# Performance work log

Hardware: AMD Instinct MI355X
Metric: run time of the kernel (lower is better)

Reference implementation:

```python
import jax, jax.numpy as jnp
import numpy as np

D_MODEL = 2048
D_STATE = 128
D_CONV = 4
NHEADS = 64
NGROUPS = 1
HEAD_DIM = 64
CHUNK = 128
EPS = 1e-5
D_INNER = NHEADS * HEAD_DIM                       # 4096
CONV_DIM = D_INNER + 2 * NGROUPS * D_STATE        # 4352
D_IN_PROJ = 2 * D_INNER + 2 * NGROUPS * D_STATE + NHEADS  # 8512


def setup_inputs() -> dict:
    key = jax.random.key(0)
    ks = jax.random.split(key, 9)
    B, S = 2, 4096
    return dict(
        hidden_states=jax.random.normal(ks[0], (B, S, D_MODEL), jnp.float32),
        W_in=jax.random.normal(ks[1], (D_MODEL, D_IN_PROJ), jnp.float32) * 0.02,
        conv_w=jax.random.normal(ks[2], (CONV_DIM, D_CONV), jnp.float32) * 0.2,
        conv_b=jax.random.normal(ks[3], (CONV_DIM,), jnp.float32) * 0.1,
        # A must be negative (stable SSM): A = -exp(u), u ~ U[0,2)
        A=-jnp.exp(jax.random.uniform(ks[4], (NHEADS,), jnp.float32, 0.0, 2.0)),
        D=jax.random.normal(ks[5], (NHEADS,), jnp.float32),
        dt_bias=jax.random.normal(ks[6], (NHEADS,), jnp.float32),
        norm_w=jnp.ones((D_INNER,), jnp.float32),
        W_out=jax.random.normal(ks[7], (D_INNER, D_MODEL), jnp.float32) * 0.02,
    )


def _silu(x):
    return x * jax.nn.sigmoid(x)


def _causal_conv1d(x, w, b):
    # depthwise causal conv with silu; x [B,S,C], w [C,K], b [C]
    K = w.shape[1]
    S = x.shape[1]
    xp = jnp.pad(x, ((0, 0), (K - 1, 0), (0, 0)))
    y = sum(xp[:, k:k + S, :] * w[None, None, :, k].swapaxes(-1, -1) for k in range(0))
    y = jnp.zeros_like(x)
    for k in range(K):
        y = y + xp[:, k:k + S, :] * w[:, k][None, None, :]
    return _silu(y + b)


def _ssd(x, dt, A, Bm, Cm, chunk):
    # Mamba2 chunked SSD scan.
    # x [b,s,h,p]; dt [b,s,h] (>0); A [h]; Bm,Cm [b,s,g,n]
    b, s, h, p = x.shape
    g, n = Bm.shape[2], Bm.shape[3]
    hh = h // g
    c = s // chunk
    x = x.reshape(b, c, chunk, g, hh, p)
    dt = dt.reshape(b, c, chunk, g, hh)
    Bm = Bm.reshape(b, c, chunk, g, n)
    Cm = Cm.reshape(b, c, chunk, g, n)
    dA = dt * A.reshape(g, hh)                 # [b,c,l,g,hh]
    dA_cs = jnp.cumsum(dA, axis=2)             # [b,c,l,g,hh]
    dtx = dt[..., None] * x                    # [b,c,l,g,hh,p]
    # intra-chunk (diagonal blocks): L[i,j] = exp(sum_{j<k<=i} dA)
    diff = dA_cs[:, :, :, None] - dA_cs[:, :, None, :]   # [b,c,i,j,g,hh]
    mask = jnp.tril(jnp.ones((chunk, chunk), bool))
    L = jnp.exp(jnp.where(mask[None, None, :, :, None, None], diff, -jnp.inf))
    Y = jnp.einsum('bcign,bcjgn,bcijgh,bcjghp->bcighp', Cm, Bm, L, dtx)
    # chunk-final states
    decay = jnp.exp(dA_cs[:, :, -1:] - dA_cs)            # [b,c,l,g,hh]
    states = jnp.einsum('bcjgn,bcjgh,bcjghp->bcghpn', Bm, decay, dtx)
    chunk_decay = jnp.exp(dA_cs[:, :, -1])               # [b,c,g,hh]
    def step(prev, inp):
        cd, st = inp
        return cd[..., None, None] * prev + st, prev
    init = jnp.zeros_like(states[:, 0])
    _, prevs = jax.lax.scan(step, init,
                            (jnp.moveaxis(chunk_decay, 1, 0), jnp.moveaxis(states, 1, 0)))
    prevs = jnp.moveaxis(prevs, 0, 1)                    # [b,c,g,hh,p,n] state entering each chunk
    Y = Y + jnp.einsum('bcign,bcghpn,bcigh->bcighp', Cm, prevs, jnp.exp(dA_cs))
    return Y.reshape(b, s, h, p)


def reference(hidden_states, W_in, conv_w, conv_b, A, D, dt_bias, norm_w, W_out):
    Bsz, S, _ = hidden_states.shape
    zxbcdt = hidden_states @ W_in                        # [B,S,d_in_proj]
    z = zxbcdt[..., :D_INNER]
    xbc = zxbcdt[..., D_INNER:D_INNER + CONV_DIM]
    dt = zxbcdt[..., D_INNER + CONV_DIM:]                # [B,S,nheads]
    xbc = _causal_conv1d(xbc, conv_w, conv_b)            # silu-activated causal conv
    x = xbc[..., :D_INNER].reshape(Bsz, S, NHEADS, HEAD_DIM)
    Bm = xbc[..., D_INNER:D_INNER + NGROUPS * D_STATE].reshape(Bsz, S, NGROUPS, D_STATE)
    Cm = xbc[..., D_INNER + NGROUPS * D_STATE:].reshape(Bsz, S, NGROUPS, D_STATE)
    dt = jax.nn.softplus(dt + dt_bias)                   # delta_softplus, dt_limit=(0,inf)
    y = _ssd(x, dt, A, Bm, Cm, CHUNK)
    y = y + D[None, None, :, None] * x                   # skip (D) term
    y = y.reshape(Bsz, S, D_INNER)
    # gated RMSNorm (norm_before_gate=False): normalize(y * silu(z)), grouped
    yg = y * _silu(z)
    gsz = D_INNER // NGROUPS
    ygr = yg.reshape(Bsz, S, NGROUPS, gsz)
    rms = jax.lax.rsqrt(jnp.mean(ygr * ygr, axis=-1, keepdims=True) + EPS)
    yn = (ygr * rms).reshape(Bsz, S, D_INNER) * norm_w
    return yn @ W_out
```

## Files before the change

### kernel.cpp

```cpp
#include <hip/hip_runtime.h>
#include <hip/hip_bf16.h>

typedef __bf16 bf16_t;
typedef bf16_t bf16x8 __attribute__((ext_vector_type(8)));
typedef float f32x4 __attribute__((ext_vector_type(4)));

#define TOK 8192
#define DMODEL 2048
#define DINNER 4096
#define XBCN 4352
#define DSTATE 128
#define NH 64
#define HD 64
#define NBC 64
#define WINT_ROWS 8448

__device__ __forceinline__ void gld16(const bf16_t* g, bf16_t* l) {
  __builtin_amdgcn_global_load_lds((const __attribute__((address_space(1))) void*)g,
                                   (__attribute__((address_space(3))) void*)l, 16, 0, 0);
}

__device__ __forceinline__ f32x4 mfma16(bf16x8 a, bf16x8 b, f32x4 c) {
  return __builtin_amdgcn_mfma_f32_16x16x32_bf16(a, b, c, 0, 0, 0);
}

__device__ __forceinline__ bf16x8 ldsr(unsigned addr) {
  f32x4 r;
  asm volatile("ds_read_b128 %0, %1" : "=v"(r) : "v"(addr));
  return __builtin_bit_cast(bf16x8, r);
}


__global__ __launch_bounds__(256)
void cast_split_kernel(const float* __restrict__ in, bf16_t* __restrict__ hi,
                       bf16_t* __restrict__ lo, size_t n) {
  size_t i = ((size_t)blockIdx.x * 256 + threadIdx.x) * 8;
  if (i + 8 > n) return;
  float4 a = *(const float4*)(in + i);
  float4 b = *(const float4*)(in + i + 4);
  float v[8] = {a.x,a.y,a.z,a.w,b.x,b.y,b.z,b.w};
  bf16x8 h, l;
#pragma unroll
  for (int j = 0; j < 8; ++j) {
    h[j] = (bf16_t)v[j];
    l[j] = (bf16_t)(v[j] - (float)h[j]);
  }
  *(bf16x8*)(hi + i) = h;
  *(bf16x8*)(lo + i) = l;
}

__global__ __launch_bounds__(256)
void transpose_cast_kernel(const float* __restrict__ in, bf16_t* __restrict__ out,
                           int R, int C, int outRows) {
  __shared__ float tile[32][33];
  const int c0 = blockIdx.x * 32;
  const int r0 = blockIdx.y * 32;
  const int tx = threadIdx.x & 31;
  const int ty = threadIdx.x >> 5;
#pragma unroll
  for (int k = 0; k < 4; ++k) {
    int r = r0 + ty + k*8;
    int c = c0 + tx;
    tile[ty + k*8][tx] = (c < C) ? in[(size_t)r * C + c] : 0.f;
  }
  __syncthreads();
#pragma unroll
  for (int k = 0; k < 4; ++k) {
    int oc = c0 + ty + k*8;
    int orr = r0 + tx;
    out[(size_t)oc * R + orr] = (bf16_t)tile[tx][ty + k*8];
  }
}

__global__ __launch_bounds__(256)
void wdt_split_kernel(const float* __restrict__ Win, bf16_t* __restrict__ Whi,
                      bf16_t* __restrict__ Wlo) {
  const int h = threadIdx.x & 63;
  const int k0 = blockIdx.x * 256 + (threadIdx.x >> 6) * 64;
#pragma unroll 4
  for (int i = 0; i < 64; ++i) {
    int k = k0 + i;
    float v = Win[(size_t)k * 8512 + 8448 + h];
    bf16_t hv = (bf16_t)v;
    Whi[(size_t)h * DMODEL + k] = hv;
    Wlo[(size_t)h * DMODEL + k] = (bf16_t)(v - (float)hv);
  }
}

template <typename OutT>
__global__ __launch_bounds__(512, 2)
void gemm256(const bf16_t* __restrict__ A, const bf16_t* __restrict__ B,
             OutT* __restrict__ C0, OutT* __restrict__ C1,
             long M, long N, long K, long splitN, int gridX) {
  __shared__ bf16_t sA[2][2][8192];
  __shared__ bf16_t sB[2][2][8192];
  const int tid = threadIdx.x;
  const int lane = tid & 63;
  const int wid = tid >> 6;
  const int wr = wid >> 2;
  const int wc = wid & 3;

  const int x = blockIdx.x & 7;
  const int q = blockIdx.x >> 3;
  const long bm = (long)(x * 4 + (q & 3)) * 256;
  const long bn = (long)(q >> 2) * 256;

  const int srow = (wid >> 1) * 16 + (lane & 15);
  const int skof = (wid & 1) * 32 + (lane >> 4) * 8;
  const bf16_t* Abase = A + (bm + srow) * K + skof;
  const bf16_t* Bbase = B + (bn + srow) * K + skof;

  auto stageA = [&](int buf, int h, long kt) {
    const bf16_t* s = Abase + (long)h * 128 * K + kt;
    gld16(s,          &sA[buf][h][wid * 512]);
    gld16(s + 64 * K, &sA[buf][h][4096 + wid * 512]);
  };
  auto stageB = [&](int buf, int h, long kt) {
    const bf16_t* s = Bbase + (long)h * 128 * K + kt;
    gld16(s,          &sB[buf][h][wid * 512]);
    gld16(s + 64 * K, &sB[buf][h][4096 + wid * 512]);
  };

  const unsigned sAb = (unsigned)(uintptr_t)(__attribute__((address_space(3))) void*)&sA[0][0][0]
                       + (unsigned)lane * 16 + (unsigned)wr * 8192;
  const unsigned sBb = (unsigned)(uintptr_t)(__attribute__((address_space(3))) void*)&sB[0][0][0]
                       + (unsigned)lane * 16 + (unsigned)wc * 4096;

  stageA(0, 0, 0); stageB(0, 0, 0); stageB(0, 1, 0); stageA(0, 1, 0);

  f32x4 acc[8][4] = {};
  bf16x8 a0[4][2], a1[4][2], b0[2][2], b1[2][2];
  int cur = 0;
  const int NT = (int)(K >> 6);

  for (int t = 0; t < NT; ++t) {
    const bool fin = (t == NT - 1);
    const long ktn = (long)(t + 1) * 64;
    const unsigned ab = sAb + (unsigned)cur * 32768;
    const unsigned bb = sBb + (unsigned)cur * 32768;

    asm volatile("s_waitcnt vmcnt(0)\n\ts_barrier" ::: "memory");

    if (!fin) {
      stageA(cur ^ 1, 0, ktn);
      stageB(cur ^ 1, 0, ktn);
      stageB(cur ^ 1, 1, ktn);
      stageA(cur ^ 1, 1, ktn);
    }
    __builtin_amdgcn_sched_barrier(0);

#pragma unroll
    for (int mi = 0; mi < 4; ++mi) {
      a0[mi][0] = ldsr(ab + (mi*2+0)*1024);
      a0[mi][1] = ldsr(ab + (mi*2+1)*1024);
    }
#pragma unroll
    for (int ni = 0; ni < 2; ++ni) {
      b0[ni][0] = ldsr(bb + (ni*2+0)*1024);
      b0[ni][1] = ldsr(bb + (ni*2+1)*1024);
    }
#pragma unroll
    for (int ni = 0; ni < 2; ++ni) {
      b1[ni][0] = ldsr(bb + 16384 + (ni*2+0)*1024);
      b1[ni][1] = ldsr(bb + 16384 + (ni*2+1)*1024);
    }
#pragma unroll
    for (int mi = 0; mi < 4; ++mi) {
      a1[mi][0] = ldsr(ab + 16384 + (mi*2+0)*1024);
      a1[mi][1] = ldsr(ab + 16384 + (mi*2+1)*1024);
    }
    __builtin_amdgcn_sched_barrier(0);

    asm volatile("s_waitcnt lgkmcnt(12)" ::: "memory");
    __builtin_amdgcn_sched_barrier(0);
    __builtin_amdgcn_s_setprio(1);
#pragma unroll
    for (int mi = 0; mi < 4; ++mi)
#pragma unroll
      for (int ni = 0; ni < 2; ++ni) {
        acc[mi][ni] = mfma16(a0[mi][0], b0[ni][0], acc[mi][ni]);
        acc[mi][ni] = mfma16(a0[mi][1], b0[ni][1], acc[mi][ni]);
      }
    __builtin_amdgcn_s_setprio(0);
    __builtin_amdgcn_sched_barrier(0);

    asm volatile("s_waitcnt lgkmcnt(8)" ::: "memory");
    __builtin_amdgcn_sched_barrier(0);
    __builtin_amdgcn_s_setprio(1);
#pragma unroll
    for (int mi = 0; mi < 4; ++mi)
#pragma unroll
      for (int ni = 0; ni < 2; ++ni) {
        acc[mi][2 + ni] = mfma16(a0[mi][0], b1[ni][0], acc[mi][2 + ni]);
        acc[mi][2 + ni] = mfma16(a0[mi][1], b1[ni][1], acc[mi][2 + ni]);
      }
    __builtin_amdgcn_s_setprio(0);
    __builtin_amdgcn_sched_barrier(0);

    asm volatile("s_waitcnt lgkmcnt(0)" ::: "memory");
    __builtin_amdgcn_sched_barrier(0);
    __builtin_amdgcn_s_setprio(1);
#pragma unroll
    for (int mi = 0; mi < 4; ++mi)
#pragma unroll
      for (int ni = 0; ni < 2; ++ni) {
        acc[4 + mi][2 + ni] = mfma16(a1[mi][0], b1[ni][0], acc[4 + mi][2 + ni]);
        acc[4 + mi][2 + ni] = mfma16(a1[mi][1], b1[ni][1], acc[4 + mi][2 + ni]);
      }
#pragma unroll
    for (int mi = 0; mi < 4; ++mi)
#pragma unroll
      for (int ni = 0; ni < 2; ++ni) {
        acc[4 + mi][ni] = mfma16(a1[mi][0], b0[ni][0], acc[4 + mi][ni]);
        acc[4 + mi][ni] = mfma16(a1[mi][1], b0[ni][1], acc[4 + mi][ni]);
      }
    __builtin_amdgcn_s_setprio(0);
    __builtin_amdgcn_sched_barrier(0);
    cur ^= 1;
  }

  const int cr = (lane >> 4) * 4;
  const int cc = lane & 15;
  OutT* Cb;
  long col0, ldc;
  if (bn < splitN) { Cb = C0; col0 = bn; ldc = splitN; }
  else             { Cb = C1; col0 = bn - splitN; ldc = N - splitN; }
#pragma unroll
  for (int mi = 0; mi < 8; ++mi) {
    long row = bm + (mi >> 2) * 128 + wr * 64 + (mi & 3) * 16 + cr;
#pragma unroll
    for (int ni = 0; ni < 4; ++ni) {
      long col = col0 + (ni >> 1) * 128 + wc * 32 + (ni & 1) * 16 + cc;
      OutT* p = Cb + row * ldc + col;
#pragma unroll
      for (int r = 0; r < 4; ++r) p[(long)r * ldc] = (OutT)acc[mi][ni][r];
    }
  }
}

__global__ __launch_bounds__(256)
void dt_mfma_kernel(const bf16_t* __restrict__ Ahi, const bf16_t* __restrict__ Alo,
                    const bf16_t* __restrict__ Whi, const bf16_t* __restrict__ Wlo,
                    float* __restrict__ dtraw) {
  __shared__ bf16_t sAh[4096], sAl[4096], sBh[2048], sBl[2048];
  const int tid = threadIdx.x;
  const int lane = tid & 63;
  const int w = tid >> 6;
  const long bm = (long)blockIdx.x * 128;
  const int rlo = lane & 15;
  const int kq = lane >> 4;

  const bf16_t* Ah0 = Ahi + (bm + 2*w*16 + rlo) * (long)DMODEL + kq*8;
  const bf16_t* Ah1 = Ah0 + 16*(long)DMODEL;
  const bf16_t* Al0 = Alo + (bm + 2*w*16 + rlo) * (long)DMODEL + kq*8;
  const bf16_t* Al1 = Al0 + 16*(long)DMODEL;
  const bf16_t* Bh0 = Whi + (w*16 + rlo) * (long)DMODEL + kq*8;
  const bf16_t* Bl0 = Wlo + (w*16 + rlo) * (long)DMODEL + kq*8;

  f32x4 acc[2][4] = {};

  for (int kt = 0; kt < DMODEL; kt += 32) {
    __syncthreads();
    gld16(Ah0 + kt, &sAh[(2*w)*512]);
    gld16(Ah1 + kt, &sAh[(2*w+1)*512]);
    gld16(Al0 + kt, &sAl[(2*w)*512]);
    gld16(Al1 + kt, &sAl[(2*w+1)*512]);
    gld16(Bh0 + kt, &sBh[w*512]);
    gld16(Bl0 + kt, &sBl[w*512]);
    __syncthreads();
    bf16x8 ah[2], al[2], bh[4], bl[4];
#pragma unroll
    for (int i = 0; i < 2; ++i) {
      ah[i] = *(const bf16x8*)&sAh[((2*w + i)*64 + lane)*8];
      al[i] = *(const bf16x8*)&sAl[((2*w + i)*64 + lane)*8];
    }
#pragma unroll
    for (int n = 0; n < 4; ++n) {
      bh[n] = *(const bf16x8*)&sBh[(n*64 + lane)*8];
      bl[n] = *(const bf16x8*)&sBl[(n*64 + lane)*8];
    }
#pragma unroll
    for (int mi = 0; mi < 2; ++mi)
#pragma unroll
      for (int n = 0; n < 4; ++n) {
        acc[mi][n] = mfma16(ah[mi], bh[n], acc[mi][n]);
        acc[mi][n] = mfma16(ah[mi], bl[n], acc[mi][n]);
        acc[mi][n] = mfma16(al[mi], bh[n], acc[mi][n]);
      }
  }

  const int cr = (lane >> 4) * 4;
  const int cc = lane & 15;
#pragma unroll
  for (int mi = 0; mi < 2; ++mi)
#pragma unroll
    for (int n = 0; n < 4; ++n)
#pragma unroll
      for (int r = 0; r < 4; ++r)
        dtraw[(bm + 2*w*16 + mi*16 + cr + r) * 64 + n*16 + cc] = acc[mi][n][r];
}

__global__ __launch_bounds__(256)
void conv_kernel(const bf16_t* __restrict__ xbc, const float* __restrict__ cw,
                 const float* __restrict__ cb, bf16_t* __restrict__ xo,
                 bf16_t* __restrict__ Bout, bf16_t* __restrict__ Cout) {
  const int c = blockIdx.x * 256 + threadIdx.x;
  const int t0 = blockIdx.y * 8;
  const int bstart = (t0 >> 12) << 12;
  const float w0 = cw[c*4+0], w1 = cw[c*4+1], w2 = cw[c*4+2], w3 = cw[c*4+3];
  const float bias = cb[c];
  float in[11];
#pragma unroll
  for (int k = 0; k < 11; ++k) {
    int t = t0 - 3 + k;
    in[k] = (t >= bstart) ? (float)xbc[(size_t)t * XBCN + c] : 0.f;
  }
#pragma unroll
  for (int i = 0; i < 8; ++i) {
    float v = bias + w0*in[i] + w1*in[i+1] + w2*in[i+2] + w3*in[i+3];
    float s = v / (1.f + __expf(-v));
    int t = t0 + i;
    bf16_t o = (bf16_t)s;
    if (c < DINNER)           xo[(size_t)t * DINNER + c] = o;
    else if (c < DINNER+128)  Bout[(size_t)t * DSTATE + (c - DINNER)] = o;
    else                      Cout[(size_t)t * DSTATE + (c - DINNER - 128)] = o;
  }
}

__global__ __launch_bounds__(256)
void dt_scan_kernel(const float* __restrict__ dtraw, const float* __restrict__ dt_bias,
                    const float* __restrict__ Avec, float* __restrict__ dt_s,
                    float* __restrict__ dAcs, float* __restrict__ cdec) {
  const int wid = blockIdx.x * 4 + (threadIdx.x >> 6);
  const int lane = threadIdx.x & 63;
  const int h = wid & 63;
  const int bc = wid >> 6;
  const long tok0 = (long)bc * 128;
  const float Ah = Avec[h];
  const float bias = dt_bias[h];
  float v0 = dtraw[(tok0 + lane)*64 + h] + bias;
  float v1 = dtraw[(tok0 + 64 + lane)*64 + h] + bias;
  float d0 = (v0 > 20.f) ? v0 : log1pf(expf(v0));
  float d1 = (v1 > 20.f) ? v1 : log1pf(expf(v1));
  float s0 = d0 * Ah;
  float s1 = d1 * Ah;
#pragma unroll
  for (int off = 1; off < 64; off <<= 1) {
    float t = __shfl_up(s0, off);
    if (lane >= off) s0 += t;
  }
  float tot0 = __shfl(s0, 63);
#pragma unroll
  for (int off = 1; off < 64; off <<= 1) {
    float t = __shfl_up(s1, off);
    if (lane >= off) s1 += t;
  }
  s1 += tot0;
  const size_t base = (size_t)wid * 128;
  dt_s[base + lane] = d0;
  dt_s[base + 64 + lane] = d1;
  dAcs[base + lane] = s0;
  dAcs[base + 64 + lane] = s1;
  if (lane == 63) cdec[wid] = __expf(s1);
}

__global__ __launch_bounds__(256)
void states_kernel(const bf16_t* __restrict__ x, const bf16_t* __restrict__ Bm,
                   const float* __restrict__ dt_s, const float* __restrict__ dAcs,
                   bf16_t* __restrict__ states) {
  __shared__ bf16_t sDtx[8192];
  __shared__ bf16_t sBd[16384];
  __shared__ float sDt[128];
  __shared__ float sDec[128];
  const int wid = blockIdx.x;
  const int h = wid & 63;
  const int bc = wid >> 6;
  const int tid = threadIdx.x;
  const int lane = tid & 63;
  const int w = tid >> 6;
  const long tok0 = (long)bc * 128;
  const size_t dbase = (size_t)wid * 128;

  if (tid < 128) {
    sDt[tid] = dt_s[dbase + tid];
  } else {
    int j = tid - 128;
    sDec[j] = __expf(dAcs[dbase + 127] - dAcs[dbase + j]);
  }
  __syncthreads();

  {
    const int jj0 = tid >> 3;
    const int pg = (tid & 7) * 8;
#pragma unroll
    for (int t = 0; t < 4; ++t) {
      int j = t*32 + jj0;
      bf16x8 xv = *(const bf16x8*)&x[(tok0 + j)*(long)DINNER + h*64 + pg];
      float dtj = sDt[j];
      int kq = (j >> 5) * 4;
      int qe = ((j >> 3) & 3) * 16;
      int e = j & 7;
#pragma unroll
      for (int i = 0; i < 8; ++i) {
        int p = pg + i;
        sDtx[((kq + (p>>4))*64 + qe + (p&15))*8 + e] = (bf16_t)((float)xv[i]*dtj);
      }
    }
    const int jj1 = tid >> 4;
    const int ng = (tid & 15) * 8;
#pragma unroll
    for (int t = 0; t < 8; ++t) {
      int j = t*16 + jj1;
      bf16x8 bv = *(const bf16x8*)&Bm[(tok0 + j)*(long)DSTATE + ng];
      float dec = sDec[j];
      int kq = (j >> 5) * 8;
      int qe = ((j >> 3) & 3) * 16;
      int e = j & 7;
#pragma unroll
      for (int i = 0; i < 8; ++i) {
        int n = ng + i;
        sBd[((kq + (n>>4))*64 + qe + (n&15))*8 + e] = (bf16_t)((float)bv[i]*dec);
      }
    }
  }
  __syncthreads();

  f32x4 acc[4][2] = {};
#pragma unroll
  for (int kt = 0; kt < 4; ++kt) {
    bf16x8 aF[4], bF[2];
#pragma unroll
    for (int mt = 0; mt < 4; ++mt) aF[mt] = *(const bf16x8*)&sDtx[((kt*4 + mt)*64 + lane)*8];
#pragma unroll
    for (int nt = 0; nt < 2; ++nt) bF[nt] = *(const bf16x8*)&sBd[((kt*8 + w*2 + nt)*64 + lane)*8];
#pragma unroll
    for (int mt = 0; mt < 4; ++mt)
#pragma unroll
      for (int nt = 0; nt < 2; ++nt)
        acc[mt][nt] = mfma16(aF[mt], bF[nt], acc[mt][nt]);
  }

  bf16_t* S = states + (size_t)wid * (HD * DSTATE);
  const int cr = (lane >> 4) * 4;
  const int cc = lane & 15;
#pragma unroll
  for (int mt = 0; mt < 4; ++mt)
#pragma unroll
    for (int nt = 0; nt < 2; ++nt) {
      int n = (w*2 + nt)*16 + cc;
#pragma unroll
      for (int r = 0; r < 4; ++r) {
        int p = mt*16 + cr + r;
        S[(size_t)p*DSTATE + n] = (bf16_t)acc[mt][nt][r];
      }
    }
}

__global__ __launch_bounds__(256)
void scan_kernel(bf16_t* __restrict__ sp, const float* __restrict__ cdec) {
  const size_t gid = (size_t)blockIdx.x * 256 + threadIdx.x;
  const int n = gid & 127;
  const int p = (gid >> 7) & 63;
  const int h = (gid >> 13) & 63;
  const int b = (int)(gid >> 19);
  float prev = 0.f;
  const size_t pn = (size_t)p * 128 + n;
  for (int c = 0; c < 32; ++c) {
    const int wid = (b*32 + c)*64 + h;
    const size_t idx = (size_t)wid * 8192 + pn;
    float s = (float)sp[idx];
    sp[idx] = (bf16_t)prev;
    prev = cdec[wid] * prev + s;
  }
}

__global__ __launch_bounds__(256)
void ssd_y_kernel(bf16_t* __restrict__ xy, const bf16_t* __restrict__ Bm,
                  const bf16_t* __restrict__ Cm, const bf16_t* __restrict__ prevs,
                  const float* __restrict__ dt_s, const float* __restrict__ dAcs,
                  const float* __restrict__ Dvec) {
  __shared__ bf16_t sG[16384];
  __shared__ bf16_t sDtx[8192];
  __shared__ float sDA[128];
  __shared__ float sEA[128];
  __shared__ float sDt[128];

  const int wid = blockIdx.x;
  const int h = wid & 63;
  const int bc = wid >> 6;
  const int tid = threadIdx.x;
  const int lane = tid & 63;
  const int w = tid >> 6;
  const long tok0 = (long)bc * 128;
  const size_t dbase = (size_t)wid * 128;

  if (tid < 128) {
    float v = dAcs[dbase + tid];
    sDA[tid] = v;
    sEA[tid] = __expf(v);
  } else {
    sDt[tid - 128] = dt_s[dbase + tid - 128];
  }
  __syncthreads();

  {
    const int jj0 = tid >> 3;
    const int pg = (tid & 7) * 8;
#pragma unroll
    for (int t = 0; t < 4; ++t) {
      int j = t*32 + jj0;
      bf16x8 xv = *(const bf16x8*)&xy[(tok0 + j)*(long)DINNER + h*64 + pg];
      float dtj = sDt[j];
      int kq = (j >> 5) * 4;
      int qe = ((j >> 3) & 3) * 16;
      int e = j & 7;
#pragma unroll
      for (int i = 0; i < 8; ++i) {
        int p = pg + i;
        sDtx[((kq + (p>>4))*64 + qe + (p&15))*8 + e] = (bf16_t)((float)xv[i]*dtj);
      }
    }
  }

  const int arow = (w*2)*16 + (lane & 15);
  const int koff = (lane >> 4) * 8;
  bf16x8 aCm[2][4];
#pragma unroll
  for (int mi = 0; mi < 2; ++mi)
#pragma unroll
    for (int kt = 0; kt < 4; ++kt)
      aCm[mi][kt] = *(const bf16x8*)&Cm[(tok0 + arow + mi*16)*(long)DSTATE + kt*32 + koff];

  const bf16_t* P = prevs + (size_t)wid * 8192;
  f32x4 accY[2][4] = {};
#pragma unroll
  for (int kt = 0; kt < 4; ++kt) {
    bf16x8 bP[4];
#pragma unroll
    for (int ni = 0; ni < 4; ++ni)
      bP[ni] = *(const bf16x8*)&P[(size_t)(ni*16 + (lane & 15))*DSTATE + kt*32 + koff];
#pragma unroll
    for (int mi = 0; mi < 2; ++mi)
#pragma unroll
      for (int ni = 0; ni < 4; ++ni)
        accY[mi][ni] = mfma16(aCm[mi][kt], bP[ni], accY[mi][ni]);
  }
  const int cr = (lane >> 4) * 4;
  const int cc = lane & 15;
#pragma unroll
  for (int mi = 0; mi < 2; ++mi)
#pragma unroll
    for (int r = 0; r < 4; ++r) {
      float e = sEA[(w*2 + mi)*16 + cr + r];
#pragma unroll
      for (int ni = 0; ni < 4; ++ni) accY[mi][ni][r] *= e;
    }

  f32x4 accS[2][8] = {};
#pragma unroll
  for (int kt = 0; kt < 4; ++kt) {
    bf16x8 bB[8];
#pragma unroll
    for (int nt = 0; nt < 8; ++nt)
      bB[nt] = *(const bf16x8*)&Bm[(tok0 + nt*16 + (lane & 15))*(long)DSTATE + kt*32 + koff];
#pragma unroll
    for (int mi = 0; mi < 2; ++mi)
#pragma unroll
      for (int nt = 0; nt < 8; ++nt)
        accS[mi][nt] = mfma16(aCm[mi][kt], bB[nt], accS[mi][nt]);
  }

#pragma unroll
  for (int mi = 0; mi < 2; ++mi)
#pragma unroll
    for (int nt = 0; nt < 8; ++nt)
#pragma unroll
      for (int r = 0; r < 4; ++r) {
        int i = (w*2 + mi)*16 + cr + r;
        int j = nt*16 + cc;
        float g = (i >= j) ? accS[mi][nt][r] * __expf(sDA[i] - sDA[j]) : 0.f;
        sG[(((j>>5)*8 + (i>>4))*64 + ((j>>3)&3)*16 + (i&15))*8 + (j&7)] = (bf16_t)g;
      }
  __syncthreads();

#pragma unroll
  for (int kt = 0; kt < 4; ++kt) {
    bf16x8 aG[2], bD[4];
#pragma unroll
    for (int mi = 0; mi < 2; ++mi) aG[mi] = *(const bf16x8*)&sG[((kt*8 + w*2 + mi)*64 + lane)*8];
#pragma unroll
    for (int ni = 0; ni < 4; ++ni) bD[ni] = *(const bf16x8*)&sDtx[((kt*4 + ni)*64 + lane)*8];
#pragma unroll
    for (int mi = 0; mi < 2; ++mi)
#pragma unroll
      for (int ni = 0; ni < 4; ++ni)
        accY[mi][ni] = mfma16(aG[mi], bD[ni], accY[mi][ni]);
  }

  const float Dh = Dvec[h];
#pragma unroll
  for (int mi = 0; mi < 2; ++mi)
#pragma unroll
    for (int ni = 0; ni < 4; ++ni)
#pragma unroll
      for (int r = 0; r < 4; ++r) {
        long tokr = tok0 + (w*2 + mi)*16 + cr + r;
        int p = ni*16 + cc;
        long idx = tokr * DINNER + h*64 + p;
        float xv = (float)xy[idx];
        xy[idx] = (bf16_t)(accY[mi][ni][r] + Dh * xv);
      }
}

__global__ __launch_bounds__(256)
void gate_kernel(const bf16_t* __restrict__ y, const bf16_t* __restrict__ z,
                 const float* __restrict__ norm_w, bf16_t* __restrict__ yn) {
  const int tok = blockIdx.x;
  const int tid = threadIdx.x;
  const int lane = tid & 63;
  const int w = tid >> 6;
  const bf16_t* yrow = y + (size_t)tok * DINNER;
  const bf16_t* zrow = z + (size_t)tok * DINNER;
  float local[16];
  float ss = 0.f;
#pragma unroll
  for (int v = 0; v < 2; ++v) {
    int col = tid*16 + v*8;
    bf16x8 yv = *(const bf16x8*)&yrow[col];
    bf16x8 zv = *(const bf16x8*)&zrow[col];
#pragma unroll
    for (int i = 0; i < 8; ++i) {
      float zf = (float)zv[i];
      float g = zf / (1.f + __expf(-zf));
      float t = (float)yv[i] * g;
      local[v*8 + i] = t;
      ss += t*t;
    }
  }
#pragma unroll
  for (int off = 32; off > 0; off >>= 1) ss += __shfl_xor(ss, off);
  __shared__ float red[4];
  if (lane == 0) red[w] = ss;
  __syncthreads();
  float rms = rsqrtf((red[0]+red[1]+red[2]+red[3]) * (1.f/DINNER) + 1e-5f);
  bf16_t* orow = yn + (size_t)tok * DINNER;
#pragma unroll
  for (int v = 0; v < 2; ++v) {
    int col = tid*16 + v*8;
    bf16x8 o;
#pragma unroll
    for (int i = 0; i < 8; ++i) o[i] = (bf16_t)(local[v*8+i] * rms * norm_w[col+i]);
    *(bf16x8*)&orow[col] = o;
  }
}

extern "C" void kernel_launch(void* const* d_in, const int* in_sizes, int n_in,
                              void* d_out, int out_size, void* d_ws, size_t ws_size,
                              hipStream_t stream) {
  const float* hidden  = (const float*)d_in[0];
  const float* W_in    = (const float*)d_in[1];
  const float* conv_w  = (const float*)d_in[2];
  const float* conv_b  = (const float*)d_in[3];
  const float* Avec    = (const float*)d_in[4];
  const float* Dvec    = (const float*)d_in[5];
  const float* dt_bias = (const float*)d_in[6];
  const float* norm_w  = (const float*)d_in[7];
  const float* W_out   = (const float*)d_in[8];

  char* ws = (char*)d_ws;
  size_t off = 0;
  auto take = [&](size_t bytes) -> char* {
    char* p = ws + off;
    off += (bytes + 255) & ~(size_t)255;
    return p;
  };
  bf16_t* R1    = (bf16_t*)take((size_t)NBC * NH * HD * DSTATE * 2);
  bf16_t* WinT  = (bf16_t*)take((size_t)WINT_ROWS * DMODEL * 2);
  bf16_t* xbc   = (bf16_t*)take((size_t)TOK * XBCN * 2);
  bf16_t* xconv = (bf16_t*)take((size_t)TOK * DINNER * 2);
  bf16_t* Bmat  = (bf16_t*)take((size_t)TOK * DSTATE * 2);
  bf16_t* Cmat  = (bf16_t*)take((size_t)TOK * DSTATE * 2);
  float*  dtraw = (float*)take((size_t)TOK * NH * 4);
  float*  dt_s  = (float*)take((size_t)TOK * NH * 4);
  float*  dAcs  = (float*)take((size_t)TOK * NH * 4);
  float*  cdec  = (float*)take((size_t)NBC * NH * 4);
  bf16_t* Wdth  = (bf16_t*)take((size_t)NH * DMODEL * 2);
  bf16_t* Wdtl  = (bf16_t*)take((size_t)NH * DMODEL * 2);
  if (off > ws_size) return;

  bf16_t* Xb      = R1;
  bf16_t* Xlo     = xbc;
  bf16_t* statesB = R1;
  bf16_t* ynbuf   = R1;
  bf16_t* WoutT   = WinT;
  bf16_t* zbuf    = (bf16_t*)d_out;
  float*  out     = (float*)d_out;

  cast_split_kernel<<<(TOK*DMODEL)/2048, 256, 0, stream>>>(hidden, Xb, Xlo, (size_t)TOK*DMODEL);
  wdt_split_kernel<<<DMODEL/256, 256, 0, stream>>>(W_in, Wdth, Wdtl);
  dt_mfma_kernel<<<TOK/128, 256, 0, stream>>>(Xb, Xlo, Wdth, Wdtl, dtraw);
  transpose_cast_kernel<<<dim3(WINT_ROWS/32, DMODEL/32), 256, 0, stream>>>(W_in, WinT, DMODEL, 8512, WINT_ROWS);
  gemm256<bf16_t><<<(TOK/256)*(WINT_ROWS/256), 512, 0, stream>>>(
      Xb, WinT, zbuf, xbc, TOK, WINT_ROWS, DMODEL, DINNER, WINT_ROWS/256);
  transpose_cast_kernel<<<dim3(DMODEL/32, DINNER/32), 256, 0, stream>>>(W_out, WoutT, DINNER, DMODEL, DMODEL);
  conv_kernel<<<dim3(XBCN/256, TOK/8), 256, 0, stream>>>(xbc, conv_w, conv_b, xconv, Bmat, Cmat);
  dt_scan_kernel<<<(NBC*NH)/4, 256, 0, stream>>>(dtraw, dt_bias, Avec, dt_s, dAcs, cdec);
  states_kernel<<<NBC*NH, 256, 0, stream>>>(xconv, Bmat, dt_s, dAcs, statesB);
  scan_kernel<<<(NBC*NH*HD*DSTATE)/(32*256), 256, 0, stream>>>(statesB, cdec);
  ssd_y_kernel<<<NBC*NH, 256, 0, stream>>>(xconv, Bmat, Cmat, statesB, dt_s, dAcs, Dvec);
  gate_kernel<<<TOK, 256, 0, stream>>>(xconv, zbuf, norm_w, ynbuf);
  gemm256<float><<<(TOK/256)*(DMODEL/256), 512, 0, stream>>>(
      ynbuf, WoutT, out, out, TOK, DMODEL, DINNER, DMODEL, DMODEL/256);
}
```

Before: 1.041 ms.

## Interleave staged loads with MFMA quadrants in gemm256 and retile dt GEMM

The main bf16 GEMM loop now splits each K-step into four MFMA quadrants. Each quadrant's half-tile global-to-LDS stage and its LDS fragment reads are interleaved with partial vmcnt waits and barriers, and the next tile's a0/b0 fragments are prefetched at the end of the current step. This replaces one full vmcnt(0) barrier followed by all loads, aiming to overlap memory traffic with matrix math. Separately, the split-precision dt GEMM moves to 32-row blocks of 512 threads with double-buffered LDS, one fragment per wave, and more blocks in flight. The finer-grained waitcnt accounting is fragile and adds more barriers per iteration.

```diff
diff --git a/kernel.cpp b/kernel.cpp
--- a/kernel.cpp
+++ b/kernel.cpp
@@ -86,6 +86,31 @@
     Wlo[(size_t)h * DMODEL + k] = (bf16_t)(v - (float)hv);
   }
 }
+
+#define RD_A(arr, base) \
+  _Pragma("unroll") \
+  for (int mi = 0; mi < 4; ++mi) { \
+    arr[mi][0] = ldsr((base) + (mi*2+0)*1024); \
+    arr[mi][1] = ldsr((base) + (mi*2+1)*1024); \
+  }
+
+#define RD_B(arr, base) \
+  _Pragma("unroll") \
+  for (int ni = 0; ni < 2; ++ni) { \
+    arr[ni][0] = ldsr((base) + (ni*2+0)*1024); \
+    arr[ni][1] = ldsr((base) + (ni*2+1)*1024); \
+  }
+
+#define MMAQ(MB, NB, aa, bb2) \
+  _Pragma("unroll") \
+  for (int mi = 0; mi < 4; ++mi) \
+    _Pragma("unroll") \
+    for (int ni = 0; ni < 2; ++ni) { \
+      acc[(MB)+mi][(NB)+ni] = mfma16(aa[mi][0], bb2[ni][0], acc[(MB)+mi][(NB)+ni]); \
+      acc[(MB)+mi][(NB)+ni] = mfma16(aa[mi][1], bb2[ni][1], acc[(MB)+mi][(NB)+ni]); \
+    }
+
+#define SBAR() __builtin_amdgcn_sched_barrier(0)
 
 template <typename OutT>
 __global__ __launch_bounds__(512, 2)
@@ -126,96 +151,69 @@
   const unsigned sBb = (unsigned)(uintptr_t)(__attribute__((address_space(3))) void*)&sB[0][0][0]
                        + (unsigned)lane * 16 + (unsigned)wc * 4096;
 
-  stageA(0, 0, 0); stageB(0, 0, 0); stageB(0, 1, 0); stageA(0, 1, 0);
-
+  stageA(0, 0, 0); stageB(0, 0, 0);
+  SBAR();
+  asm volatile("s_waitcnt vmcnt(0)\n\ts_barrier" ::: "memory");
   f32x4 acc[8][4] = {};
   bf16x8 a0[4][2], a1[4][2], b0[2][2], b1[2][2];
+  RD_A(a0, sAb);
+  RD_B(b0, sBb);
+  stageB(0, 1, 0); stageA(0, 1, 0);
+  SBAR();
+
   int cur = 0;
   const int NT = (int)(K >> 6);
 
   for (int t = 0; t < NT; ++t) {
     const bool fin = (t == NT - 1);
     const long ktn = (long)(t + 1) * 64;
-    const unsigned ab = sAb + (unsigned)cur * 32768;
-    const unsigned bb = sBb + (unsigned)cur * 32768;
-
-    asm volatile("s_waitcnt vmcnt(0)\n\ts_barrier" ::: "memory");
-
+    const unsigned ab  = sAb + (unsigned)cur * 32768;
+    const unsigned bb  = sBb + (unsigned)cur * 32768;
+    const unsigned abn = sAb + (unsigned)(cur ^ 1) * 32768;
+    const unsigned bbn = sBb + (unsigned)(cur ^ 1) * 32768;
+
+    asm volatile("s_waitcnt vmcnt(2)\n\ts_barrier" ::: "memory");
+    if (!fin) stageA(cur ^ 1, 0, ktn);
+    RD_B(b1, bb + 16384);
+    asm volatile("s_waitcnt lgkmcnt(4)" ::: "memory");
+    SBAR();
+    __builtin_amdgcn_s_setprio(1);
+    MMAQ(0, 0, a0, b0);
+    __builtin_amdgcn_s_setprio(0);
+    SBAR();
+
+    if (!fin) asm volatile("s_waitcnt vmcnt(2)\n\ts_barrier" ::: "memory");
+    else      asm volatile("s_waitcnt vmcnt(0)\n\ts_barrier" ::: "memory");
+    if (!fin) stageB(cur ^ 1, 0, ktn);
+    RD_A(a1, ab + 16384);
+    asm volatile("s_waitcnt lgkmcnt(8)" ::: "memory");
+    SBAR();
+    __builtin_amdgcn_s_setprio(1);
+    MMAQ(0, 2, a0, b1);
+    __builtin_amdgcn_s_setprio(0);
+    SBAR();
+
+    asm volatile("s_barrier" ::: "memory");
+    if (!fin) stageB(cur ^ 1, 1, ktn);
+    asm volatile("s_waitcnt lgkmcnt(0)" ::: "memory");
+    SBAR();
+    __builtin_amdgcn_s_setprio(1);
+    MMAQ(4, 0, a1, b0);
+    __builtin_amdgcn_s_setprio(0);
+    SBAR();
+
+    if (!fin) asm volatile("s_waitcnt vmcnt(2)\n\ts_barrier" ::: "memory");
+    else      asm volatile("s_barrier" ::: "memory");
     if (!fin) {
-      stageA(cur ^ 1, 0, ktn);
-      stageB(cur ^ 1, 0, ktn);
-      stageB(cur ^ 1, 1, ktn);
       stageA(cur ^ 1, 1, ktn);
-    }
-    __builtin_amdgcn_sched_barrier(0);
-
-#pragma unroll
-    for (int mi = 0; mi < 4; ++mi) {
-      a0[mi][0] = ldsr(ab + (mi*2+0)*1024);
-      a0[mi][1] = ldsr(ab + (mi*2+1)*1024);
-    }
-#pragma unroll
-    for (int ni = 0; ni < 2; ++ni) {
-      b0[ni][0] = ldsr(bb + (ni*2+0)*1024);
-      b0[ni][1] = ldsr(bb + (ni*2+1)*1024);
-    }
-#pragma unroll
-    for (int ni = 0; ni < 2; ++ni) {
-      b1[ni][0] = ldsr(bb + 16384 + (ni*2+0)*1024);
-      b1[ni][1] = ldsr(bb + 16384 + (ni*2+1)*1024);
-    }
-#pragma unroll
-    for (int mi = 0; mi < 4; ++mi) {
-      a1[mi][0] = ldsr(ab + 16384 + (mi*2+0)*1024);
-      a1[mi][1] = ldsr(ab + 16384 + (mi*2+1)*1024);
-    }
-    __builtin_amdgcn_sched_barrier(0);
-
-    asm volatile("s_waitcnt lgkmcnt(12)" ::: "memory");
-    __builtin_amdgcn_sched_barrier(0);
+      RD_A(a0, abn);
+      RD_B(b0, bbn);
+    }
+    SBAR();
     __builtin_amdgcn_s_setprio(1);
-#pragma unroll
-    for (int mi = 0; mi < 4; ++mi)
-#pragma unroll
-      for (int ni = 0; ni < 2; ++ni) {
-        acc[mi][ni] = mfma16(a0[mi][0], b0[ni][0], acc[mi][ni]);
-        acc[mi][ni] = mfma16(a0[mi][1], b0[ni][1], acc[mi][ni]);
-      }
+    MMAQ(4, 2, a1, b1);
     __builtin_amdgcn_s_setprio(0);
-    __builtin_amdgcn_sched_barrier(0);
-
-    asm volatile("s_waitcnt lgkmcnt(8)" ::: "memory");
-    __builtin_amdgcn_sched_barrier(0);
-    __builtin_amdgcn_s_setprio(1);
-#pragma unroll
-    for (int mi = 0; mi < 4; ++mi)
-#pragma unroll
-      for (int ni = 0; ni < 2; ++ni) {
-        acc[mi][2 + ni] = mfma16(a0[mi][0], b1[ni][0], acc[mi][2 + ni]);
-        acc[mi][2 + ni] = mfma16(a0[mi][1], b1[ni][1], acc[mi][2 + ni]);
-      }
-    __builtin_amdgcn_s_setprio(0);
-    __builtin_amdgcn_sched_barrier(0);
-
-    asm volatile("s_waitcnt lgkmcnt(0)" ::: "memory");
-    __builtin_amdgcn_sched_barrier(0);
-    __builtin_amdgcn_s_setprio(1);
-#pragma unroll
-    for (int mi = 0; mi < 4; ++mi)
-#pragma unroll
-      for (int ni = 0; ni < 2; ++ni) {
-        acc[4 + mi][2 + ni] = mfma16(a1[mi][0], b1[ni][0], acc[4 + mi][2 + ni]);
-        acc[4 + mi][2 + ni] = mfma16(a1[mi][1], b1[ni][1], acc[4 + mi][2 + ni]);
-      }
-#pragma unroll
-    for (int mi = 0; mi < 4; ++mi)
-#pragma unroll
-      for (int ni = 0; ni < 2; ++ni) {
-        acc[4 + mi][ni] = mfma16(a1[mi][0], b0[ni][0], acc[4 + mi][ni]);
-        acc[4 + mi][ni] = mfma16(a1[mi][1], b0[ni][1], acc[4 + mi][ni]);
-      }
-    __builtin_amdgcn_s_setprio(0);
-    __builtin_amdgcn_sched_barrier(0);
+    SBAR();
     cur ^= 1;
   }
 
@@ -238,66 +236,55 @@
   }
 }
 
-__global__ __launch_bounds__(256)
+__global__ __launch_bounds__(512)
 void dt_mfma_kernel(const bf16_t* __restrict__ Ahi, const bf16_t* __restrict__ Alo,
                     const bf16_t* __restrict__ Whi, const bf16_t* __restrict__ Wlo,
                     float* __restrict__ dtraw) {
-  __shared__ bf16_t sAh[4096], sAl[4096], sBh[2048], sBl[2048];
+  __shared__ bf16_t sb[2][6144];
   const int tid = threadIdx.x;
   const int lane = tid & 63;
   const int w = tid >> 6;
-  const long bm = (long)blockIdx.x * 128;
+  const long bm = (long)blockIdx.x * 32;
   const int rlo = lane & 15;
   const int kq = lane >> 4;
-
-  const bf16_t* Ah0 = Ahi + (bm + 2*w*16 + rlo) * (long)DMODEL + kq*8;
-  const bf16_t* Ah1 = Ah0 + 16*(long)DMODEL;
-  const bf16_t* Al0 = Alo + (bm + 2*w*16 + rlo) * (long)DMODEL + kq*8;
-  const bf16_t* Al1 = Al0 + 16*(long)DMODEL;
-  const bf16_t* Bh0 = Whi + (w*16 + rlo) * (long)DMODEL + kq*8;
-  const bf16_t* Bl0 = Wlo + (w*16 + rlo) * (long)DMODEL + kq*8;
-
-  f32x4 acc[2][4] = {};
-
-  for (int kt = 0; kt < DMODEL; kt += 32) {
+  const long K = DMODEL;
+
+  const bf16_t* srcA  = (w < 2 ? Ahi : Alo) + (bm + (w & 1) * 16 + rlo) * K + kq * 8;
+  const bf16_t* srcBl = Wlo + ((w & 3) * 16 + rlo) * K + kq * 8;
+  const bf16_t* srcBh = Whi + (((w - 4) & 3) * 16 + rlo) * K + kq * 8;
+
+  auto stage = [&](int b, long kt) {
+    if (w < 4) {
+      gld16(srcA + kt,  &sb[b][w * 512]);
+      gld16(srcBl + kt, &sb[b][4096 + w * 512]);
+    } else {
+      gld16(srcBh + kt, &sb[b][2048 + (w - 4) * 512]);
+    }
+  };
+
+  const int mfrag = w >> 2;
+  const int nfrag = w & 3;
+  f32x4 acc = {};
+  stage(0, 0);
+  __syncthreads();
+  int cur = 0;
+  for (long kt = 0; kt < K; kt += 32) {
+    if (kt + 32 < K) stage(cur ^ 1, kt + 32);
+    bf16x8 ah = *(const bf16x8*)&sb[cur][mfrag * 512 + lane * 8];
+    bf16x8 al = *(const bf16x8*)&sb[cur][1024 + mfrag * 512 + lane * 8];
+    bf16x8 bh = *(const bf16x8*)&sb[cur][2048 + nfrag * 512 + lane * 8];
+    bf16x8 bl = *(const bf16x8*)&sb[cur][4096 + nfrag * 512 + lane * 8];
+    acc = mfma16(ah, bh, acc);
+    acc = mfma16(ah, bl, acc);
+    acc = mfma16(al, bh, acc);
     __syncthreads();
-    gld16(Ah0 + kt, &sAh[(2*w)*512]);
-    gld16(Ah1 + kt, &sAh[(2*w+1)*512]);
-    gld16(Al0 + kt, &sAl[(2*w)*512]);
-    gld16(Al1 + kt, &sAl[(2*w+1)*512]);
-    gld16(Bh0 + kt, &sBh[w*512]);
-    gld16(Bl0 + kt, &sBl[w*512]);
-    __syncthreads();
-    bf16x8 ah[2], al[2], bh[4], bl[4];
-#pragma unroll
-    for (int i = 0; i < 2; ++i) {
-      ah[i] = *(const bf16x8*)&sAh[((2*w + i)*64 + lane)*8];
-      al[i] = *(const bf16x8*)&sAl[((2*w + i)*64 + lane)*8];
-    }
-#pragma unroll
-    for (int n = 0; n < 4; ++n) {
-      bh[n] = *(const bf16x8*)&sBh[(n*64 + lane)*8];
-      bl[n] = *(const bf16x8*)&sBl[(n*64 + lane)*8];
-    }
-#pragma unroll
-    for (int mi = 0; mi < 2; ++mi)
-#pragma unroll
-      for (int n = 0; n < 4; ++n) {
-        acc[mi][n] = mfma16(ah[mi], bh[n], acc[mi][n]);
-        acc[mi][n] = mfma16(ah[mi], bl[n], acc[mi][n]);
-        acc[mi][n] = mfma16(al[mi], bh[n], acc[mi][n]);
-      }
-  }
-
+    cur ^= 1;
+  }
   const int cr = (lane >> 4) * 4;
   const int cc = lane & 15;
 #pragma unroll
-  for (int mi = 0; mi < 2; ++mi)
-#pragma unroll
-    for (int n = 0; n < 4; ++n)
-#pragma unroll
-      for (int r = 0; r < 4; ++r)
-        dtraw[(bm + 2*w*16 + mi*16 + cr + r) * 64 + n*16 + cc] = acc[mi][n][r];
+  for (int r = 0; r < 4; ++r)
+    dtraw[(bm + mfrag * 16 + cr + r) * 64 + nfrag * 16 + cc] = acc[r];
 }
 
 __global__ __launch_bounds__(256)
@@ -698,7 +685,7 @@
 
   cast_split_kernel<<<(TOK*DMODEL)/2048, 256, 0, stream>>>(hidden, Xb, Xlo, (size_t)TOK*DMODEL);
   wdt_split_kernel<<<DMODEL/256, 256, 0, stream>>>(W_in, Wdth, Wdtl);
-  dt_mfma_kernel<<<TOK/128, 256, 0, stream>>>(Xb, Xlo, Wdth, Wdtl, dtraw);
+  dt_mfma_kernel<<<TOK/32, 512, 0, stream>>>(Xb, Xlo, Wdth, Wdtl, dtraw);
   transpose_cast_kernel<<<dim3(WINT_ROWS/32, DMODEL/32), 256, 0, stream>>>(W_in, WinT, DMODEL, 8512, WINT_ROWS);
   gemm256<bf16_t><<<(TOK/256)*(WINT_ROWS/256), 512, 0, stream>>>(
       Xb, WinT, zbuf, xbc, TOK, WINT_ROWS, DMODEL, DINNER, WINT_ROWS/256);
```

Measured after the change: 953.3 us. -8.4%, faster.
